# Optimization experiments

Hardware: AMD Instinct MI355X
Metric: run time of the kernel (lower is better)

The kernel has to match this reference:

```python
import jax, jax.numpy as jnp
import numpy as np

H = 32        # num_heads
E = 128       # hidden_dim (per-head K/V/query dim)
D_STATE = 512 # encoder state width
B, LQ, LK = 8, 1024, 1024


def setup_inputs() -> dict:
    key = jax.random.key(0)
    ks = jax.random.split(key, 8)
    query = jax.random.normal(ks[0], (B, LQ, E), dtype=jnp.float32)
    states = jax.random.normal(ks[1], (B, LK, D_STATE), dtype=jnp.float32)
    s = 1.0 / np.sqrt(D_STATE)
    Wk = jax.random.uniform(ks[2], (H, D_STATE, E), minval=-s, maxval=s, dtype=jnp.float32)
    bk = jax.random.uniform(ks[3], (H, E), minval=-s, maxval=s, dtype=jnp.float32)
    Wv = jax.random.uniform(ks[4], (H, D_STATE, E), minval=-s, maxval=s, dtype=jnp.float32)
    bv = jax.random.uniform(ks[5], (H, E), minval=-s, maxval=s, dtype=jnp.float32)
    so = 1.0 / np.sqrt(H * E)
    Wo = jax.random.uniform(ks[6], (H * E, E), minval=-so, maxval=so, dtype=jnp.float32)
    bo = jax.random.uniform(ks[7], (E,), minval=-so, maxval=so, dtype=jnp.float32)
    return {"query": query, "states": states, "Wk": Wk, "bk": bk,
            "Wv": Wv, "bv": bv, "Wo": Wo, "bo": bo}


def reference(query, states, Wk, bk, Wv, bv, Wo, bo):
    # Per-head K/V projections of the shared states: [H,B,Lk,E]
    keys = jnp.einsum('bkd,hde->hbke', states, Wk) + bk[:, None, None, :]
    values = jnp.einsum('bkd,hde->hbke', states, Wv) + bv[:, None, None, :]
    # Scaled dot-product scores: [H,B,Lq,Lk]
    scale = 1.0 / jnp.sqrt(jnp.asarray(E, dtype=query.dtype))
    scores = jnp.einsum('bqe,hbke->hbqk', query, keys) * scale
    # Original detaches the softmax output before AV
    attn = jax.lax.stop_gradient(jax.nn.softmax(scores, axis=-1))
    ctx = jnp.einsum('hbqk,hbke->hbqe', attn, values)       # [H,B,Lq,E]
    # concat heads along last dim: [B,Lq,H*E]
    ctx = jnp.transpose(ctx, (1, 2, 0, 3)).reshape(query.shape[0], query.shape[1], -1)
    return ctx @ Wo + bo
```

## Files before the change

kernel.cpp:

```cpp
#include <hip/hip_runtime.h>

#define H_  32
#define E_  128
#define D_  512
#define B_  8
#define LQ_ 1024
#define LK_ 1024

typedef __bf16 bf16x8 __attribute__((ext_vector_type(8)));
typedef float  f32x4  __attribute__((ext_vector_type(4)));
typedef float  f32x16 __attribute__((ext_vector_type(16)));

typedef __attribute__((address_space(1))) const unsigned int guint;
typedef __attribute__((address_space(3))) unsigned int luint;

__device__ __forceinline__ f32x4 MFMA16(bf16x8 a, bf16x8 b, f32x4 c) {
    return __builtin_amdgcn_mfma_f32_16x16x32_bf16(a, b, c, 0, 0, 0);
}
__device__ __forceinline__ f32x16 MFMA32(bf16x8 a, bf16x8 b, f32x16 c) {
    return __builtin_amdgcn_mfma_f32_32x32x16_bf16(a, b, c, 0, 0, 0);
}

__device__ __forceinline__ unsigned short f2bf(float x) {
    union { float f; unsigned u; } v; v.f = x;
    unsigned r = v.u + 0x7fffu + ((v.u >> 16) & 1u);
    return (unsigned short)(r >> 16);
}
__device__ __forceinline__ unsigned pkbf(float a, float b) {
    union { float f; unsigned u; } x, y; x.f = a; y.f = b;
    return __builtin_amdgcn_perm(y.u, x.u, 0x07060302u);
}

__global__ void conv_scale_kernel(const float* __restrict__ in,
                                  unsigned short* __restrict__ out,
                                  long n4, float scale) {
    long i = blockIdx.x * (long)blockDim.x + threadIdx.x;
    long stride = (long)gridDim.x * blockDim.x;
    for (; i < n4; i += stride) {
        float4 v = ((const float4*)in)[i];
        union { unsigned long long u; unsigned short s[4]; } p;
        p.s[0] = f2bf(v.x * scale); p.s[1] = f2bf(v.y * scale);
        p.s[2] = f2bf(v.z * scale); p.s[3] = f2bf(v.w * scale);
        ((unsigned long long*)out)[i] = p.u;
    }
}

__global__ void transpose_bf16_kernel(const float* __restrict__ in,
                                      unsigned short* __restrict__ out,
                                      int R, int C, long inStride, long outStride) {
    in  += (long)blockIdx.z * inStride;
    out += (long)blockIdx.z * outStride;
    __shared__ float t[32][33];
    int x = threadIdx.x, y = threadIdx.y;
    int c0 = blockIdx.x * 32, r0 = blockIdx.y * 32;
    for (int i = 0; i < 32; i += 8) t[y + i][x] = in[(long)(r0 + y + i) * C + (c0 + x)];
    __syncthreads();
    for (int i = 0; i < 32; i += 8)
        out[(long)(c0 + y + i) * R + (r0 + x)] = f2bf(t[x][y + i]);
}

__global__ __launch_bounds__(512, 4) void kv_proj_kernel(
    const unsigned short* __restrict__ sb,
    const unsigned short* __restrict__ wkt,
    const unsigned short* __restrict__ wvt,
    const float* __restrict__ bk, const float* __restrict__ bv,
    unsigned short* __restrict__ Kb,
    unsigned short* __restrict__ Vtb)
{
    int bid = blockIdx.x;
    const int x  = bid & 7;  int s = bid >> 3;
    const int hh = s & 3;    s >>= 2;
    const int kv = s & 1;    s >>= 1;
    const int mt = s & 3;    s >>= 2;
    const int b  = s;
    const int h  = hh * 8 + x;

    const unsigned short* wt = kv ? wvt : wkt;
    const float* bias = kv ? bv : bk;

    __shared__ unsigned short As[2][256 * 32];
    __shared__ unsigned short Bs[2][128 * 32];

    const int tid = threadIdx.x;
    const int wave = tid >> 6, lane = tid & 63;
    const int ln = lane & 31, hi = lane >> 5;
    const int wm = wave & 3, wn = wave >> 2;

    const unsigned short* Ag = sb + ((long)b * LK_ + mt * 256) * D_;
    const unsigned short* Bg = wt + (long)h * E_ * D_;

    int aoff[2], boff;
    #pragma unroll
    for (int d = 0; d < 2; d++) {
        int row = (wave * 2 + d) * 16 + (lane >> 2);
        int ch  = (lane & 3) ^ ((row >> 1) & 3);
        aoff[d] = row * D_ + ch * 8;
    }
    {
        int row = wave * 16 + (lane >> 2);
        int ch  = (lane & 3) ^ ((row >> 1) & 3);
        boff = row * D_ + ch * 8;
    }

    #define KV_STAGE(d0_, buf_)                                                     \
        do {                                                                        \
            _Pragma("unroll")                                                       \
            for (int d = 0; d < 2; d++)                                             \
                __builtin_amdgcn_global_load_lds(                                   \
                    (guint*)(Ag + aoff[d] + (d0_)),                                 \
                    (luint*)&As[buf_][(wave * 2 + d) * 512], 16, 0, 0);             \
            __builtin_amdgcn_global_load_lds(                                       \
                (guint*)(Bg + boff + (d0_)),                                        \
                (luint*)&Bs[buf_][wave * 512], 16, 0, 0);                           \
        } while (0)

    KV_STAGE(0, 0);
    __syncthreads();

    f32x16 acc[4] = {};

    for (int it = 0; it < 16; it++) {
        const int buf = it & 1;
        if (it < 15) KV_STAGE((it + 1) * 32, buf ^ 1);

        #pragma unroll
        for (int ss = 0; ss < 2; ss++) {
            const int c = ss * 2 + hi;
            bf16x8 af[2], bfr[2];
            #pragma unroll
            for (int mb = 0; mb < 2; mb++) {
                const int r = wm * 64 + mb * 32 + ln;
                af[mb] = *(const bf16x8*)&As[buf][r * 32 + (c ^ ((r >> 1) & 3)) * 8];
            }
            #pragma unroll
            for (int nb = 0; nb < 2; nb++) {
                const int r = wn * 64 + nb * 32 + ln;
                bfr[nb] = *(const bf16x8*)&Bs[buf][r * 32 + (c ^ ((r >> 1) & 3)) * 8];
            }
            #pragma unroll
            for (int mb = 0; mb < 2; mb++)
                #pragma unroll
                for (int nb = 0; nb < 2; nb++)
                    acc[mb * 2 + nb] = MFMA32(af[mb], bfr[nb], acc[mb * 2 + nb]);
        }
        __syncthreads();
    }

    const int row0 = mt * 256 + wm * 64;
    const int e0 = wn * 64;
    if (!kv) {
        const long base = ((long)h * B_ + b) * LK_;
        #pragma unroll
        for (int mb = 0; mb < 2; mb++)
            #pragma unroll
            for (int nb = 0; nb < 2; nb++) {
                const int e = e0 + nb * 32 + ln;
                const float be = bias[h * E_ + e];
                #pragma unroll
                for (int r = 0; r < 16; r++) {
                    int row = row0 + mb * 32 + (r & 3) + 8 * (r >> 2) + 4 * hi;
                    Kb[(base + row) * E_ + e] = f2bf(acc[mb * 2 + nb][r] + be);
                }
            }
    } else {
        const long vbase = ((long)h * B_ + b) * E_;
        #pragma unroll
        for (int mb = 0; mb < 2; mb++)
            #pragma unroll
            for (int nb = 0; nb < 2; nb++) {
                const int e = e0 + nb * 32 + ln;
                const float be = bias[h * E_ + e];
                #pragma unroll
                for (int rg = 0; rg < 4; rg++) {
                    int k0 = row0 + mb * 32 + 8 * rg + 4 * hi;
                    union { unsigned long long u; unsigned short s2[4]; } pk;
                    #pragma unroll
                    for (int j = 0; j < 4; j++)
                        pk.s2[j] = f2bf(acc[mb * 2 + nb][rg * 4 + j] + be);
                    *(unsigned long long*)&Vtb[(vbase + e) * (long)LK_ + k0] = pk.u;
                }
            }
    }
}

__global__ __launch_bounds__(256, 3) void attn_kernel(
    const unsigned short* __restrict__ qb,
    const unsigned short* __restrict__ Kb,
    const unsigned short* __restrict__ Vtb,
    unsigned short* __restrict__ ctx)
{
    int bid = blockIdx.x;
    const int b = bid & 7;
    int s = bid >> 3;
    const int qt = s & 7;
    const int h  = s >> 3;

    __shared__ unsigned short Ks[64 * 128];
    __shared__ unsigned short Vs[2][128 * 64];

    const int tid = threadIdx.x;
    const int wave = tid >> 6, lane = tid & 63;
    const int ln = lane & 31, hi = lane >> 5;

    const unsigned short* Kg = Kb  + ((long)h * B_ + b) * (long)LK_ * E_;
    const unsigned short* Vg = Vtb + ((long)h * B_ + b) * (long)E_ * LK_;
    const int qrow = qt * 128 + wave * 32;

    bf16x8 qf[8];
    #pragma unroll
    for (int s8 = 0; s8 < 8; s8++) {
        union { uint4 u; bf16x8 v; } t;
        t.u = *(const uint4*)&qb[((long)b * LQ_ + qrow + ln) * E_ + s8 * 16 + hi * 8];
        qf[s8] = t.v;
    }

    int koff[4], voff[4];
    #pragma unroll
    for (int d = 0; d < 4; d++) {
        int krow = (wave * 4 + d) * 4 + (lane >> 4);
        int kc = (lane & 15) ^ (krow & 15);
        koff[d] = krow * E_ + kc * 8;
        int vrow = (wave * 4 + d) * 8 + (lane >> 3);
        int vc = (lane & 7) ^ (vrow & 7);
        voff[d] = vrow * LK_ + vc * 8;
    }

    #define STAGE_K(t_)                                                             \
        do {                                                                        \
            _Pragma("unroll")                                                       \
            for (int d = 0; d < 4; d++)                                             \
                __builtin_amdgcn_global_load_lds(                                   \
                    (guint*)(Kg + (long)(t_) * (64 * E_) + koff[d]),                \
                    (luint*)&Ks[(wave * 4 + d) * 512], 16, 0, 0);                   \
        } while (0)
    #define STAGE_V(t_, buf_)                                                       \
        do {                                                                        \
            _Pragma("unroll")                                                       \
            for (int d = 0; d < 4; d++)                                             \
                __builtin_amdgcn_global_load_lds(                                   \
                    (guint*)(Vg + (t_) * 64 + voff[d]),                             \
                    (luint*)&Vs[buf_][(wave * 4 + d) * 512], 16, 0, 0);             \
        } while (0)

    STAGE_K(0);
    STAGE_V(0, 0);
    __syncthreads();

    f32x16 O[4] = {};
    float l_run = 0.f;

    for (int t = 0; t < 16; t++) {
        const int vb = t & 1;

        f32x16 S[2] = {};
        #pragma unroll
        for (int es = 0; es < 8; es++) {
            #pragma unroll
            for (int mb = 0; mb < 2; mb++) {
                const int row = mb * 32 + ln;
                const int cs = (es * 2 + hi) ^ (row & 15);
                bf16x8 kf = *(const bf16x8*)&Ks[row * 128 + cs * 8];
                S[mb] = MFMA32(kf, qf[es], S[mb]);
            }
        }

        __syncthreads();
        if (t < 15) {
            STAGE_K(t + 1);
            STAGE_V(t + 1, vb ^ 1);
        }

        float tsum = 0.f;
        #pragma unroll
        for (int mb = 0; mb < 2; mb++) {
            float pv[16];
            #pragma unroll
            for (int r = 0; r < 16; r++) {
                pv[r] = __builtin_amdgcn_exp2f(S[mb][r]);
                tsum += pv[r];
            }
            unsigned a0 = pkbf(pv[0],  pv[1]),  b0 = pkbf(pv[2],  pv[3]);
            unsigned a1 = pkbf(pv[4],  pv[5]),  b1 = pkbf(pv[6],  pv[7]);
            unsigned a2 = pkbf(pv[8],  pv[9]),  b2 = pkbf(pv[10], pv[11]);
            unsigned a3 = pkbf(pv[12], pv[13]), b3 = pkbf(pv[14], pv[15]);
            unsigned r0 = __shfl_xor(hi ? a0 : a1, 32, 64);
            unsigned r1 = __shfl_xor(hi ? b0 : b1, 32, 64);
            unsigned r2 = __shfl_xor(hi ? a2 : a3, 32, 64);
            unsigned r3 = __shfl_xor(hi ? b2 : b3, 32, 64);
            #pragma unroll
            for (int st = 0; st < 2; st++) {
                union { unsigned u[4]; bf16x8 v; } pa;
                if (st == 0) {
                    pa.u[0] = hi ? r0 : a0;  pa.u[1] = hi ? r1 : b0;
                    pa.u[2] = hi ? a1 : r0;  pa.u[3] = hi ? b1 : r1;
                } else {
                    pa.u[0] = hi ? r2 : a2;  pa.u[1] = hi ? r3 : b2;
                    pa.u[2] = hi ? a3 : r2;  pa.u[3] = hi ? b3 : r3;
                }
                #pragma unroll
                for (int nb = 0; nb < 4; nb++) {
                    const int vrow = nb * 32 + ln;
                    const int vc = (mb * 4 + st * 2 + hi) ^ (vrow & 7);
                    bf16x8 vf = *(const bf16x8*)&Vs[vb][vrow * 64 + vc * 8];
                    O[nb] = MFMA32(pa.v, vf, O[nb]);
                }
            }
        }
        tsum += __shfl_xor(tsum, 32, 64);
        l_run += tsum;

        __syncthreads();
    }

    const float linv = 1.f / l_run;
    #pragma unroll
    for (int r = 0; r < 16; r++) {
        const int rowmap = (r & 3) + 8 * (r >> 2) + 4 * hi;
        float lv = __shfl(linv, rowmap, 64);
        int qg = qrow + rowmap;
        long rowbase = ((long)b * LQ_ + qg) * (H_ * E_) + h * E_;
        #pragma unroll
        for (int nb = 0; nb < 4; nb++)
            ctx[rowbase + nb * 32 + ln] = f2bf(O[nb][r] * lv);
    }
}

__global__ __launch_bounds__(512) void out_proj_kernel(
    const unsigned short* __restrict__ ctx,
    const unsigned short* __restrict__ wot,
    const float* __restrict__ bo,
    float* __restrict__ out)
{
    const int qt = blockIdx.x;
    __shared__ unsigned short As[2][32 * 128];
    __shared__ unsigned short Bs[2][128 * 128];

    const int tid = threadIdx.x;
    const int wave = tid >> 6, lane = tid & 63;
    const int l16 = lane & 15, l4 = lane >> 4;
    const int wm = wave >> 2, wn = wave & 3;

    const unsigned short* Ag = ctx + (long)(qt * 32) * (H_ * E_);

    long goff[5]; int isB[5], dbase[5];
    #pragma unroll
    for (int i = 0; i < 5; i++) {
        int d  = wave * 5 + i;
        int bB = (d >= 8);
        int dd = bB ? d - 8 : d;
        int r  = dd * 4 + l4;
        int sc = l16 ^ (r & 7);
        goff[i]  = (long)r * (H_ * E_) + sc * 8;
        isB[i]   = bB;
        dbase[i] = dd * 512;
    }

    #define OP_STAGE(k0_, buf_)                                                     \
        do {                                                                        \
            _Pragma("unroll")                                                       \
            for (int i = 0; i < 5; i++) {                                           \
                if (isB[i])                                                         \
                    __builtin_amdgcn_global_load_lds(                               \
                        (guint*)(wot + goff[i] + (k0_)),                            \
                        (luint*)&Bs[buf_][dbase[i]], 16, 0, 0);                     \
                else                                                                \
                    __builtin_amdgcn_global_load_lds(                               \
                        (guint*)(Ag + goff[i] + (k0_)),                             \
                        (luint*)&As[buf_][dbase[i]], 16, 0, 0);                     \
            }                                                                       \
        } while (0)

    OP_STAGE(0, 0);
    __syncthreads();

    f32x4 acc[2] = {};

    for (int kt = 0; kt < 32; kt++) {
        const int buf = kt & 1;
        if (kt < 31) OP_STAGE((kt + 1) * 128, buf ^ 1);

        const int ar = wm * 16 + l16;
        #pragma unroll
        for (int ks = 0; ks < 4; ks++) {
            const int sl = ks * 4 + l4;
            bf16x8 af = *(const bf16x8*)&As[buf][ar * 128 + (sl ^ (ar & 7)) * 8];
            #pragma unroll
            for (int nb = 0; nb < 2; nb++) {
                const int br = wn * 32 + nb * 16 + l16;
                bf16x8 bf = *(const bf16x8*)&Bs[buf][br * 128 + (sl ^ (br & 7)) * 8];
                acc[nb] = MFMA16(af, bf, acc[nb]);
            }
        }
        __syncthreads();
    }

    #pragma unroll
    for (int nb = 0; nb < 2; nb++) {
        const int e = wn * 32 + nb * 16 + l16;
        const float be = bo[e];
        #pragma unroll
        for (int r = 0; r < 4; r++) {
            int m = qt * 32 + wm * 16 + l4 * 4 + r;
            out[(long)m * E_ + e] = acc[nb][r] + be;
        }
    }
}

extern "C" void kernel_launch(void* const* d_in, const int* in_sizes, int n_in,
                              void* d_out, int out_size, void* d_ws, size_t ws_size,
                              hipStream_t stream) {
    const float* query  = (const float*)d_in[0];
    const float* states = (const float*)d_in[1];
    const float* Wk     = (const float*)d_in[2];
    const float* bk     = (const float*)d_in[3];
    const float* Wv     = (const float*)d_in[4];
    const float* bv     = (const float*)d_in[5];
    const float* Wo     = (const float*)d_in[6];
    const float* bo     = (const float*)d_in[7];
    float* out = (float*)d_out;

    const size_t WS_QB  = 0;
    const size_t WS_SB  = WS_QB  + 2097152UL;
    const size_t WS_WKT = WS_SB  + 8388608UL;
    const size_t WS_WVT = WS_WKT + 4194304UL;
    const size_t WS_WOT = WS_WVT + 4194304UL;
    const size_t WS_KB  = WS_WOT + 1048576UL;
    const size_t WS_VTB = WS_KB  + 67108864UL;
    const size_t WS_CTX = WS_VTB + 67108864UL;
    const size_t WS_END = WS_CTX + 67108864UL;
    if (ws_size < WS_END) return;

    char* ws = (char*)d_ws;
    unsigned short* qb  = (unsigned short*)(ws + WS_QB);
    unsigned short* sb  = (unsigned short*)(ws + WS_SB);
    unsigned short* wkt = (unsigned short*)(ws + WS_WKT);
    unsigned short* wvt = (unsigned short*)(ws + WS_WVT);
    unsigned short* wot = (unsigned short*)(ws + WS_WOT);
    unsigned short* Kb  = (unsigned short*)(ws + WS_KB);
    unsigned short* Vtb = (unsigned short*)(ws + WS_VTB);
    unsigned short* ctx = (unsigned short*)(ws + WS_CTX);

    const float SCALE = 0.12751744f;

    conv_scale_kernel<<<512, 256, 0, stream>>>(query, qb, (long)(B_ * LQ_ * E_ / 4), SCALE);
    conv_scale_kernel<<<1024, 256, 0, stream>>>(states, sb, (long)(B_ * LK_ * D_ / 4), 1.0f);
    transpose_bf16_kernel<<<dim3(4, 16, 32), dim3(32, 8), 0, stream>>>(
        Wk, wkt, D_, E_, (long)D_ * E_, (long)D_ * E_);
    transpose_bf16_kernel<<<dim3(4, 16, 32), dim3(32, 8), 0, stream>>>(
        Wv, wvt, D_, E_, (long)D_ * E_, (long)D_ * E_);
    transpose_bf16_kernel<<<dim3(4, 128, 1), dim3(32, 8), 0, stream>>>(
        Wo, wot, H_ * E_, E_, 0L, 0L);

    kv_proj_kernel<<<2048, 512, 0, stream>>>(sb, wkt, wvt, bk, bv, Kb, Vtb);
    attn_kernel<<<2048, 256, 0, stream>>>(qb, Kb, Vtb, ctx);

    out_proj_kernel<<<256, 512, 0, stream>>>(ctx, wot, bo, out);
}
```

Before: 381.7 us.

## Merge preprocessing launches into one kernel and issue V prefetch earlier in attention

Five separate conversion and transpose launches are folded into a single prep kernel that dispatches on block index, removing launch gaps between small kernels. In the attention loop, the next V tile's async load is now issued before the QK^T MFMAs. The __syncthreads is replaced by a raw s_barrier with a sched_barrier, and only the K staging stays after it, so V transfer overlaps with score computation. The raw barrier drops the implicit waitcnt that __syncthreads provides, so correctness relies on V's double buffer and existing waits elsewhere.

```diff
diff --git a/kernel.cpp b/kernel.cpp
--- a/kernel.cpp
+++ b/kernel.cpp
@@ -31,32 +31,51 @@
     return __builtin_amdgcn_perm(y.u, x.u, 0x07060302u);
 }
 
-__global__ void conv_scale_kernel(const float* __restrict__ in,
-                                  unsigned short* __restrict__ out,
-                                  long n4, float scale) {
-    long i = blockIdx.x * (long)blockDim.x + threadIdx.x;
-    long stride = (long)gridDim.x * blockDim.x;
-    for (; i < n4; i += stride) {
-        float4 v = ((const float4*)in)[i];
-        union { unsigned long long u; unsigned short s[4]; } p;
-        p.s[0] = f2bf(v.x * scale); p.s[1] = f2bf(v.y * scale);
-        p.s[2] = f2bf(v.z * scale); p.s[3] = f2bf(v.w * scale);
-        ((unsigned long long*)out)[i] = p.u;
-    }
-}
-
-__global__ void transpose_bf16_kernel(const float* __restrict__ in,
-                                      unsigned short* __restrict__ out,
-                                      int R, int C, long inStride, long outStride) {
-    in  += (long)blockIdx.z * inStride;
-    out += (long)blockIdx.z * outStride;
-    __shared__ float t[32][33];
-    int x = threadIdx.x, y = threadIdx.y;
-    int c0 = blockIdx.x * 32, r0 = blockIdx.y * 32;
-    for (int i = 0; i < 32; i += 8) t[y + i][x] = in[(long)(r0 + y + i) * C + (c0 + x)];
-    __syncthreads();
-    for (int i = 0; i < 32; i += 8)
-        out[(long)(c0 + y + i) * R + (r0 + x)] = f2bf(t[x][y + i]);
+__global__ void prep_kernel(const float* __restrict__ query,
+                            const float* __restrict__ states,
+                            const float* __restrict__ Wk,
+                            const float* __restrict__ Wv,
+                            const float* __restrict__ Wo,
+                            unsigned short* __restrict__ qb,
+                            unsigned short* __restrict__ sb,
+                            unsigned short* __restrict__ wkt,
+                            unsigned short* __restrict__ wvt,
+                            unsigned short* __restrict__ wot) {
+    const int bid = blockIdx.x;
+    const int tid = threadIdx.x;
+    if (bid < 1536) {
+        const float* in; unsigned short* out; long n4; float scale; int vb, nb;
+        if (bid < 512) { in = query;  out = qb; n4 = (long)B_ * LQ_ * E_ / 4;
+                         scale = 0.12751744f; vb = bid;       nb = 512; }
+        else           { in = states; out = sb; n4 = (long)B_ * LK_ * D_ / 4;
+                         scale = 1.0f;         vb = bid - 512; nb = 1024; }
+        long i = (long)vb * 256 + tid;
+        long stride = (long)nb * 256;
+        for (; i < n4; i += stride) {
+            float4 v = ((const float4*)in)[i];
+            union { unsigned long long u; unsigned short s[4]; } p;
+            p.s[0] = f2bf(v.x * scale); p.s[1] = f2bf(v.y * scale);
+            p.s[2] = f2bf(v.z * scale); p.s[3] = f2bf(v.w * scale);
+            ((unsigned long long*)out)[i] = p.u;
+        }
+    } else {
+        const float* in; unsigned short* out; int R, C, x, y, z; long S;
+        if (bid < 3584)      { int l = bid - 1536; in = Wk; out = wkt; R = D_; C = E_;
+                               S = (long)D_ * E_; x = l & 3; y = (l >> 2) & 15; z = l >> 6; }
+        else if (bid < 5632) { int l = bid - 3584; in = Wv; out = wvt; R = D_; C = E_;
+                               S = (long)D_ * E_; x = l & 3; y = (l >> 2) & 15; z = l >> 6; }
+        else                 { int l = bid - 5632; in = Wo; out = wot; R = H_ * E_; C = E_;
+                               S = 0;             x = l & 3; y = l >> 2;        z = 0; }
+        in  += (long)z * S;
+        out += (long)z * S;
+        __shared__ float t[32][33];
+        const int tx = tid & 31, ty = tid >> 5;
+        const int c0 = x * 32, r0 = y * 32;
+        for (int i = 0; i < 32; i += 8) t[ty + i][tx] = in[(long)(r0 + ty + i) * C + (c0 + tx)];
+        __syncthreads();
+        for (int i = 0; i < 32; i += 8)
+            out[(long)(c0 + ty + i) * R + (r0 + tx)] = f2bf(t[tx][ty + i]);
+    }
 }
 
 __global__ __launch_bounds__(512, 4) void kv_proj_kernel(
@@ -252,6 +271,8 @@
     for (int t = 0; t < 16; t++) {
         const int vb = t & 1;
 
+        if (t < 15) STAGE_V(t + 1, vb ^ 1);
+
         f32x16 S[2] = {};
         #pragma unroll
         for (int es = 0; es < 8; es++) {
@@ -264,11 +285,9 @@
             }
         }
 
-        __syncthreads();
-        if (t < 15) {
-            STAGE_K(t + 1);
-            STAGE_V(t + 1, vb ^ 1);
-        }
+        __builtin_amdgcn_s_barrier();
+        __builtin_amdgcn_sched_barrier(0);
+        if (t < 15) STAGE_K(t + 1);
 
         float tsum = 0.f;
         #pragma unroll
@@ -440,19 +459,9 @@
     unsigned short* Vtb = (unsigned short*)(ws + WS_VTB);
     unsigned short* ctx = (unsigned short*)(ws + WS_CTX);
 
-    const float SCALE = 0.12751744f;
-
-    conv_scale_kernel<<<512, 256, 0, stream>>>(query, qb, (long)(B_ * LQ_ * E_ / 4), SCALE);
-    conv_scale_kernel<<<1024, 256, 0, stream>>>(states, sb, (long)(B_ * LK_ * D_ / 4), 1.0f);
-    transpose_bf16_kernel<<<dim3(4, 16, 32), dim3(32, 8), 0, stream>>>(
-        Wk, wkt, D_, E_, (long)D_ * E_, (long)D_ * E_);
-    transpose_bf16_kernel<<<dim3(4, 16, 32), dim3(32, 8), 0, stream>>>(
-        Wv, wvt, D_, E_, (long)D_ * E_, (long)D_ * E_);
-    transpose_bf16_kernel<<<dim3(4, 128, 1), dim3(32, 8), 0, stream>>>(
-        Wo, wot, H_ * E_, E_, 0L, 0L);
-
+    prep_kernel<<<6144, 256, 0, stream>>>(query, states, Wk, Wv, Wo,
+                                          qb, sb, wkt, wvt, wot);
     kv_proj_kernel<<<2048, 512, 0, stream>>>(sb, wkt, wvt, bk, bv, Kb, Vtb);
     attn_kernel<<<2048, 256, 0, stream>>>(qb, Kb, Vtb, ctx);
-
     out_proj_kernel<<<256, 512, 0, stream>>>(ctx, wot, bo, out);
 }
```

Result: faster. 373.3 us (-2.2%).
